# Optimization experiments

Hardware: AMD Instinct MI355X
Metric: run time of the kernel (lower is better)

Reference implementation:

```python
import jax, jax.numpy as jnp
import numpy as np

B, T, E, A, S, H = 1024, 64, 1024, 10, 30, 200  # batch, time, embed, actdim, stoch, deter==hidden
MIN_STD = 0.1


def _xavier(key, fan_in, fan_out):
    lim = float(np.sqrt(6.0 / (fan_in + fan_out)))
    return jax.random.uniform(key, (fan_in, fan_out), jnp.float32, -lim, lim)


def setup_inputs() -> dict:
    key = jax.random.key(0)
    ks = jax.random.split(key, 20)
    gl = 1.0 / float(np.sqrt(H))  # torch GRUCell default init bound
    inp = {
        'embed': jax.random.normal(ks[0], (B, T, E), jnp.float32),
        'action': jax.random.normal(ks[1], (B, T, A), jnp.float32),
        'eps_post': jax.random.normal(ks[2], (T, B, S), jnp.float32),
        'eps_prior': jax.random.normal(ks[3], (T, B, S), jnp.float32),
        # Linear weights stored [in, out] (transposed vs torch) so x @ W works.
        'img1_w': _xavier(ks[4], A + S, H), 'img1_b': jnp.zeros((H,), jnp.float32),
        'gru_wi': jax.random.uniform(ks[5], (H, 3 * H), jnp.float32, -gl, gl),
        'gru_wh': jax.random.uniform(ks[6], (H, 3 * H), jnp.float32, -gl, gl),
        'gru_bi': jax.random.uniform(ks[7], (3 * H,), jnp.float32, -gl, gl),
        'gru_bh': jax.random.uniform(ks[8], (3 * H,), jnp.float32, -gl, gl),
        'img2_w': _xavier(ks[9], H, H), 'img2_b': jnp.zeros((H,), jnp.float32),
        'img3_w': _xavier(ks[10], H, 2 * S), 'img3_b': jnp.zeros((2 * S,), jnp.float32),
        'obs1_w': _xavier(ks[11], H + E, H), 'obs1_b': jnp.zeros((H,), jnp.float32),
        'obs2_w': _xavier(ks[12], H, 2 * S), 'obs2_b': jnp.zeros((2 * S,), jnp.float32),
    }
    return inp


def _observe(embed, action, eps_post, eps_prior,
             img1_w, img1_b, gru_wi, gru_wh, gru_bi, gru_bh,
             img2_w, img2_b, img3_w, img3_b, obs1_w, obs1_b, obs2_w, obs2_b):
    elu = jax.nn.elu
    embed_t = jnp.transpose(embed, (1, 0, 2))   # [T,B,E]
    action_t = jnp.transpose(action, (1, 0, 2))  # [T,B,A]

    def step(carry, xs):
        stoch, deter = carry
        a, emb, ep_q, ep_p = xs
        # img_step (prior)
        x = elu(jnp.concatenate([stoch, a], -1) @ img1_w + img1_b)
        gi = x @ gru_wi + gru_bi
        gh = deter @ gru_wh + gru_bh
        ir, iz, i_n = jnp.split(gi, 3, axis=-1)
        hr, hz, h_n = jnp.split(gh, 3, axis=-1)
        r = jax.nn.sigmoid(ir + hr)
        z = jax.nn.sigmoid(iz + hz)
        n = jnp.tanh(i_n + r * h_n)
        deter = (1.0 - z) * n + z * deter
        y = elu(deter @ img2_w + img2_b) @ img3_w + img3_b
        p_mean, p_std = jnp.split(y, 2, axis=-1)
        p_std = jax.nn.softplus(p_std) + MIN_STD
        p_stoch = p_mean + p_std * ep_p  # rsample
        # obs_step (posterior)
        o = elu(jnp.concatenate([deter, emb], -1) @ obs1_w + obs1_b) @ obs2_w + obs2_b
        q_mean, q_std = jnp.split(o, 2, axis=-1)
        q_std = jax.nn.softplus(q_std) + MIN_STD
        q_stoch = q_mean + q_std * ep_q  # rsample
        out = jnp.concatenate([q_mean, q_std, q_stoch, deter,
                               p_mean, p_std, p_stoch, deter], axis=-1)
        return (q_stoch, deter), out

    init = (jnp.zeros((B, S), embed.dtype), jnp.zeros((B, H), embed.dtype))
    _, outs = jax.lax.scan(step, init, (action_t, embed_t, eps_post, eps_prior))
    # outs: [T, B, 2*(3S+H)] -> [B, T, 580]; layout: post(mean,std,stoch,deter)|prior(mean,std,stoch,deter)
    return jnp.transpose(outs, (1, 0, 2))


def reference(embed, action, eps_post, eps_prior,
              img1_w, img1_b, gru_wi, gru_wh, gru_bi, gru_bh,
              img2_w, img2_b, img3_w, img3_b, obs1_w, obs1_b, obs2_w, obs2_b):
    return _observe(embed, action, eps_post, eps_prior,
                    img1_w, img1_b, gru_wi, gru_wh, gru_bi, gru_bh,
                    img2_w, img2_b, img3_w, img3_b, obs1_w, obs1_b, obs2_w, obs2_b)
```

## Files before the change

### kernel.cpp

```cpp
#include <hip/hip_runtime.h>

#define T_ 64

typedef __attribute__((ext_vector_type(4))) float f32x4;
typedef __attribute__((ext_vector_type(8))) short s16x8;

__device__ __forceinline__ unsigned short f2bf(float f) {
  unsigned u = __float_as_uint(f);
  u = (u + 0x7FFFu + ((u >> 16) & 1u)) >> 16;
  return (unsigned short)u;
}
__device__ __forceinline__ float bf2f(unsigned short h) {
  return __uint_as_float(((unsigned)h) << 16);
}
__device__ __forceinline__ float eluf(float x) { return x > 0.f ? x : __expf(x) - 1.f; }
__device__ __forceinline__ float sigmf(float x) { return 1.f / (1.f + __expf(-x)); }
__device__ __forceinline__ float tanh_(float x) {
  float xx = fminf(fmaxf(x, -30.f), 30.f);
  float e = __expf(-2.f * xx);
  return (1.f - e) / (1.f + e);
}
__device__ __forceinline__ float softpf(float x) {
  return x > 20.f ? x : __logf(1.f + __expf(x));
}

#define OPW1   0
#define OPWI   6656
#define OPWH   126464
#define OPO1D  246272
#define OPO2   286208
#define OPI2   298496
#define OPI3   345088
#define OWIWT  359424
#define OWHWT  364416
#define OO1DWT 369408
#define OI1WT  371072
#define OO2WT  372736
#define PK_U16 373248

#define OFF_PK  26214400
#define OFF_SWZ 26960896

__device__ void pack_mat(int idx, int stride, const float* __restrict__ W,
                         int K, int N, int KT, int NT, unsigned short* __restrict__ dst) {
  int total = KT * NT * 512;
  for (int i = idx; i < total; i += stride) {
    int j = i & 7, l = (i >> 3) & 63, rem = i >> 9;
    int kt = rem % KT, nt = rem / KT;
    int n = nt * 16 + (l & 15), k = kt * 32 + (l >> 4) * 8 + j;
    float v = (k < K && n < N) ? W[(size_t)k * N + n] : 0.f;
    dst[i] = f2bf(v);
  }
}

__device__ void pack_gate(int idx, int stride, const float* __restrict__ W,
                          unsigned short* __restrict__ dst) {
  int total = 3 * 13 * 6 * 512;
  for (int i = idx; i < total; i += stride) {
    int j = i & 7, l = (i >> 3) & 63, rem = i >> 9;
    int kt = rem % 6, rem2 = rem / 6, nt = rem2 % 13, g = rem2 / 13;
    int u = nt * 16 + (l & 15);
    int k = kt * 32 + (l >> 4) * 8 + j;
    float v = (u < 200) ? W[(size_t)k * 600 + g * 200 + u] : 0.f;
    dst[i] = f2bf(v);
  }
}

__global__ void prep_weights(const float* __restrict__ w1, const float* __restrict__ wi,
                             const float* __restrict__ wh, const float* __restrict__ i2,
                             const float* __restrict__ i3, const float* __restrict__ obs1w,
                             const float* __restrict__ o2,
                             unsigned short* __restrict__ pk,
                             unsigned short* __restrict__ swz) {
  int idx = blockIdx.x * blockDim.x + threadIdx.x;
  int stride = gridDim.x * blockDim.x;
  pack_mat(idx, stride, w1, 40, 200, 1, 13, pk + OPW1);
  pack_gate(idx, stride, wi, pk + OPWI);
  pack_gate(idx, stride, wh, pk + OPWH);
  pack_mat(idx, stride, obs1w, 200, 200, 6, 13, pk + OPO1D);
  pack_mat(idx, stride, o2, 200, 60, 6, 4, pk + OPO2);
  pack_mat(idx, stride, i2, 200, 200, 7, 13, pk + OPI2);
  pack_mat(idx, stride, i3, 200, 60, 7, 4, pk + OPI3);
  for (int i = idx; i < 4992; i += stride) {
    int j = i & 7, c = (i >> 3) % 208, g = i / 1664;
    pk[OWIWT + i] = f2bf((c < 200) ? wi[(size_t)(192 + j) * 600 + g * 200 + c] : 0.f);
    pk[OWHWT + i] = f2bf((c < 200) ? wh[(size_t)(192 + j) * 600 + g * 200 + c] : 0.f);
  }
  for (int i = idx; i < 1664; i += stride) {
    int c = i >> 3, j = i & 7;
    pk[OO1DWT + i] = f2bf((c < 200) ? obs1w[(size_t)(192 + j) * 200 + c] : 0.f);
    pk[OI1WT + i]  = f2bf((c < 200) ? w1[(size_t)(32 + j) * 200 + c] : 0.f);
  }
  for (int i = idx; i < 512; i += stride) {
    int c = i >> 3, j = i & 7;
    pk[OO2WT + i] = f2bf((c < 60) ? o2[(size_t)(192 + j) * 60 + c] : 0.f);
  }
  for (int i = idx; i < 212992; i += stride) {
    int j = i & 7, l = (i >> 3) & 63, rem = i >> 9;
    int nt = rem % 13, kc = rem / 13;
    int k = kc * 32 + ((l >> 4) * 8) + j;
    int n = nt * 16 + (l & 15);
    float v = (n < 200) ? obs1w[(size_t)(200 + k) * 200 + n] : 0.0f;
    swz[i] = f2bf(v);
  }
}

__global__ __launch_bounds__(256) void emb_gemm(const float* __restrict__ embed,
                                                const float* __restrict__ obs1b,
                                                const unsigned short* __restrict__ swz,
                                                unsigned short* __restrict__ emb_pre) {
  __shared__ __align__(16) unsigned short lds_A[64][40];
  int tid = threadIdx.x;
  int lane = tid & 63, w = tid >> 6;
  int R0 = blockIdx.x * 64;
  int tt = R0 >> 10;
  int bb = R0 & 1023;

  f32x4 acc[13];
#pragma unroll
  for (int nt = 0; nt < 13; ++nt) acc[nt] = (f32x4){0.f, 0.f, 0.f, 0.f};

  int i_row = tid >> 2, cg = tid & 3;
  const float* arow = embed + ((size_t)(bb + i_row) * 64 + tt) * 1024 + cg * 8;

  for (int kc = 0; kc < 32; ++kc) {
    __syncthreads();
    {
      const float* p = arow + kc * 32;
      f32x4 a0 = *(const f32x4*)p;
      f32x4 a1 = *(const f32x4*)(p + 4);
      unsigned short* dst = &lds_A[i_row][cg * 8];
      dst[0] = f2bf(a0[0]); dst[1] = f2bf(a0[1]); dst[2] = f2bf(a0[2]); dst[3] = f2bf(a0[3]);
      dst[4] = f2bf(a1[0]); dst[5] = f2bf(a1[1]); dst[6] = f2bf(a1[2]); dst[7] = f2bf(a1[3]);
    }
    __syncthreads();
    s16x8 af = *(const s16x8*)&lds_A[w * 16 + (lane & 15)][(lane >> 4) * 8];
    const unsigned short* bp = swz + (size_t)kc * 6656 + (size_t)lane * 8;
#pragma unroll
    for (int nt = 0; nt < 13; ++nt) {
      s16x8 bfv = *(const s16x8*)(bp + nt * 512);
      acc[nt] = __builtin_amdgcn_mfma_f32_16x16x32_bf16(af, bfv, acc[nt], 0, 0, 0);
    }
  }
  int r0 = R0 + w * 16 + ((lane >> 4) << 2);
  int c0 = lane & 15;
#pragma unroll
  for (int nt = 0; nt < 13; ++nt) {
    int n = nt * 16 + c0;
    if (n < 200) {
      float bv = obs1b[n];
#pragma unroll
      for (int rr = 0; rr < 4; ++rr)
        emb_pre[(size_t)(r0 + rr) * 200 + n] = f2bf(acc[nt][rr] + bv);
    }
  }
}

#define LGKM0  asm volatile("s_waitcnt lgkmcnt(0)" ::: "memory")
#define MEMCLB asm volatile("" ::: "memory")
#define BAR()  __builtin_amdgcn_s_barrier()
#define MFMA16(A, B, C) __builtin_amdgcn_mfma_f32_16x16x32_bf16((A), (B), (C), 0, 0, 0)
#define WV9  asm volatile("s_waitcnt vmcnt(9)" ::: "memory")
#define WV29 asm volatile("s_waitcnt vmcnt(29)" ::: "memory")
#define WV4  asm volatile("s_waitcnt vmcnt(4)" ::: "memory")
#define WV0  asm volatile("s_waitcnt vmcnt(0)" ::: "memory")

typedef __attribute__((address_space(3))) unsigned int u32_lds;
typedef const __attribute__((address_space(1))) unsigned int u32_glb;

__device__ __forceinline__ void gll16(const unsigned short* g, unsigned short* l, int lane) {
  __builtin_amdgcn_global_load_lds((u32_glb*)(g + lane * 8), (u32_lds*)l, 16, 0, 0);
}

template <int TB, bool BIGB>
__device__ __forceinline__ f32x4 cons6(const s16x8* A, f32x4 acc,
                                       unsigned short* ringw, const unsigned* toffw,
                                       const unsigned short* pk, int lane) {
#pragma unroll
  for (int kt = 0; kt < 6; ++kt) {
    const int tau = TB + kt;
    if ((tau & 3) == 0) {
      if (tau < 8) { if (BIGB) { WV29; } else { WV9; } }
      else { WV4; }
    }
    s16x8 Bv = *(const s16x8*)(ringw + (tau & 7) * 512 + lane * 8);
    acc = MFMA16(A[kt], Bv, acc);
    if ((tau & 3) == 3) {
      LGKM0; MEMCLB;
#pragma unroll
      for (int k2 = 1; k2 <= 4; ++k2) {
        const int tile = (tau + 4 + k2) % 48;
        gll16(pk + toffw[tile], ringw + (tile & 7) * 512, lane);
      }
      MEMCLB;
    }
  }
  return acc;
}

__device__ __forceinline__ f32x4 res6(const s16x8* A, const s16x8* Wt, f32x4 acc) {
#pragma unroll
  for (int kt = 0; kt < 6; ++kt) acc = MFMA16(A[kt], Wt[kt], acc);
  return acc;
}
__device__ __forceinline__ f32x4 rem1(const s16x8& A6, const unsigned short* wt,
                                      const unsigned short* zb, bool kg0, f32x4 acc) {
  const unsigned short* p = kg0 ? wt : zb;
  return MFMA16(A6, *(const s16x8*)p, acc);
}
__device__ __forceinline__ void grustep(const f32x4& rv, const f32x4& zv,
                                        const f32x4& inv, const f32x4& hnv, f32x4& dv) {
#pragma unroll
  for (int rr = 0; rr < 4; ++rr) {
    float r = sigmf(rv[rr]);
    float z = sigmf(zv[rr]);
    float n = tanh_(inv[rr] + r * hnv[rr]);
    dv[rr] = (1.f - z) * n + z * dv[rr];
  }
}

__global__ __launch_bounds__(512, 1) void scan_v7(
    const float* __restrict__ action, const float* __restrict__ eps_post,
    const float* __restrict__ img1_b, const float* __restrict__ gru_bi,
    const float* __restrict__ gru_bh, const float* __restrict__ obs2_b,
    const unsigned short* __restrict__ pk, const unsigned short* __restrict__ emb_pre,
    float* __restrict__ out) {

  __shared__ __align__(16) unsigned short ring[8][8][512];
  __shared__ __align__(16) unsigned short l_w1[13 * 512];
  __shared__ __align__(16) unsigned short l_wiWT[3][208][8];
  __shared__ __align__(16) unsigned short l_whWT[3][208][8];
  __shared__ __align__(16) unsigned short l_o1dWT[208][8];
  __shared__ __align__(16) unsigned short l_i1WT[208][8];
  __shared__ __align__(16) unsigned short l_o2WT[64][8];
  __shared__ __align__(16) unsigned short zblk[8];
  __shared__ __align__(16) unsigned short xoA[28][16][8];
  __shared__ __align__(16) unsigned short dA[28][16][8];
  __shared__ __align__(16) unsigned short sA[8][16][8];
  __shared__ __align__(16) float s_o[60][20];
  __shared__ __align__(16) float outbuf[16][292];
  __shared__ unsigned l_toff[8][48];

  const int tid = threadIdx.x, lane = tid & 63, w = tid >> 6;
  const int arow = lane & 15, kg = lane >> 4;
  const bool kg0 = (kg == 0);
  const int b0 = blockIdx.x * 16;
  unsigned short* ringw = &ring[w][0][0];
  const unsigned* toffw = &l_toff[w][0];

  for (int i = tid; i < 28 * 16 * 8; i += 512) { (&xoA[0][0][0])[i] = 0; (&dA[0][0][0])[i] = 0; }
  for (int i = tid; i < 8 * 16 * 8; i += 512) (&sA[0][0][0])[i] = 0;
  for (int i = tid; i < 13 * 512; i += 512) l_w1[i] = pk[OPW1 + i];
  for (int i = tid; i < 4992; i += 512) {
    (&l_wiWT[0][0][0])[i] = pk[OWIWT + i];
    (&l_whWT[0][0][0])[i] = pk[OWHWT + i];
  }
  for (int i = tid; i < 1664; i += 512) {
    (&l_o1dWT[0][0])[i] = pk[OO1DWT + i];
    (&l_i1WT[0][0])[i] = pk[OI1WT + i];
  }
  for (int i = tid; i < 512; i += 512) (&l_o2WT[0][0])[i] = pk[OO2WT + i];
  if (tid < 8) zblk[tid] = 0;
  for (int i = tid; i < 8 * 48; i += 512) {
    int ww = i / 48, tau = i % 48;
    unsigned off;
    if (ww < 5) {
      if (tau < 18) { int g = tau / 6, kt = tau % 6; off = OPWI + ((g * 13 + ww) * 6 + kt) * 512; }
      else {
        int t2 = tau - 18, ug = ww + 8;
        if (t2 < 6)       off = OPWI + ((0 * 13 + ug) * 6 + t2) * 512;
        else if (t2 < 12) off = OPWI + ((1 * 13 + ug) * 6 + (t2 - 6)) * 512;
        else if (t2 < 18) off = OPWH + ((1 * 13 + ug) * 6 + (t2 - 12)) * 512;
        else if (t2 < 24) off = OPWI + ((2 * 13 + ug) * 6 + (t2 - 18)) * 512;
        else              off = OPWH + ((2 * 13 + ug) * 6 + (t2 - 24)) * 512;
      }
    } else {
      if (tau < 18) { int g = tau / 6, kt = tau % 6; off = OPWI + ((g * 13 + ww) * 6 + kt) * 512; }
      else if (tau < 42) {
        int i4 = (tau - 18) / 6, kt = (tau - 18) % 6;
        int nt = (ww - 5) * 4 + i4;
        off = OPO1D + (nt * 6 + kt) * 512;
      } else {
        int kt = tau - 42;
        int nt5 = (ww == 5) ? 0 : (ww == 6) ? 1 : 3;
        off = OPO2 + (nt5 * 6 + kt) * 512;
      }
    }
    l_toff[ww][tau] = off;
  }

  s16x8 wB[4][6];
  {
    const unsigned short* base[4];
    if (w < 5) {
      base[0] = pk + OPWH + (size_t)((0 * 13 + w) * 6) * 512;
      base[1] = pk + OPWH + (size_t)((1 * 13 + w) * 6) * 512;
      base[2] = pk + OPWH + (size_t)((2 * 13 + w) * 6) * 512;
      base[3] = pk + OPWH + (size_t)((0 * 13 + w + 8) * 6) * 512;
    } else {
      base[0] = pk + OPWH + (size_t)((0 * 13 + w) * 6) * 512;
      base[1] = pk + OPWH + (size_t)((1 * 13 + w) * 6) * 512;
      base[2] = pk + OPWH + (size_t)((2 * 13 + w) * 6) * 512;
      if (w == 5)      base[3] = pk + OPO1D + (size_t)(12 * 6) * 512;
      else if (w == 7) base[3] = pk + OPO2 + (size_t)(2 * 6) * 512;
      else             base[3] = pk + OPO1D;
    }
#pragma unroll
    for (int s = 0; s < 4; ++s)
#pragma unroll
      for (int kt = 0; kt < 6; ++kt)
        wB[s][kt] = *(const s16x8*)(base[s] + (size_t)kt * 512 + lane * 8);
  }

  const int uA = w * 16 + arow;
  const int uB = (w + 8) * 16 + arow;
  const bool mB = (w < 5) && (uB < 200);
  const int uBc = (uB < 200) ? uB : 199;
  float bsA0 = gru_bi[uA] + gru_bh[uA];
  float bsA1 = gru_bi[200 + uA] + gru_bh[200 + uA];
  float bi2a = gru_bi[400 + uA], bh2a = gru_bh[400 + uA];
  float bsB0 = mB ? (gru_bi[uBc] + gru_bh[uBc]) : 0.f;
  float bsB1 = mB ? (gru_bi[200 + uBc] + gru_bh[200 + uBc]) : 0.f;
  float bi2b = mB ? gru_bi[400 + uBc] : 0.f;
  float bh2b = mB ? gru_bh[400 + uBc] : 0.f;
  float b1A = img1_b[uA];
  float b1B = mB ? img1_b[uBc] : 0.f;
  float b5a = 0.f, b5b = 0.f;
  if (w == 5) b5a = obs2_b[arow];
  else if (w == 6) b5a = obs2_b[16 + arow];
  else if (w == 7) { b5a = (48 + arow < 60) ? obs2_b[48 + arow] : 0.f; b5b = obs2_b[32 + arow]; }

  unsigned short e16[20];
#pragma unroll
  for (int i = 0; i < 20; ++i) e16[i] = 0;
  if (w >= 5) {
#pragma unroll
    for (int i = 0; i < 5; ++i) {
      int nt = (w == 5) ? ((i < 4) ? i : 12) : ((w == 6) ? (4 + ((i < 4) ? i : 3)) : (8 + ((i < 4) ? i : 3)));
      int c = nt * 16 + arow; int cc = (c < 200) ? c : 199;
#pragma unroll
      for (int rr = 0; rr < 4; ++rr)
        e16[i * 4 + rr] = emb_pre[((size_t)(b0 + kg * 4 + rr)) * 200 + cc];
    }
  }
  float epsv;
  { int it = (tid < 480) ? tid : 479;
    epsv = eps_post[((size_t)(b0 + it / 30)) * 30 + it % 30]; }
  float act0, actn;
  { int sl = (lane < 20) ? (w * 20 + lane) : (w * 20);
    act0 = action[((size_t)(b0 + sl / 10) * T_ + 0) * 10 + sl % 10];
    actn = action[((size_t)(b0 + sl / 10) * T_ + 1) * 10 + sl % 10]; }
  f32x4 dv0 = {0.f, 0.f, 0.f, 0.f}, dv1 = {0.f, 0.f, 0.f, 0.f};

  __syncthreads();
  if (lane < 20) {
    int sl = w * 20 + lane; int kk = sl % 10, r = sl / 10;
    sA[(30 + kk) >> 3][r][(30 + kk) & 7] = f2bf(act0);
  }
#pragma unroll
  for (int tt = 0; tt < 8; ++tt) gll16(pk + toffw[tt], ringw + tt * 512, lane);
  WV0;
  __syncthreads();

  for (int t = 0; t < T_; ++t) {
    {
      s16x8 a0 = *(const s16x8*)&sA[kg][arow][0];
      s16x8 a1 = *(const s16x8*)&sA[4 + kg][arow][0];
      {
        s16x8 B0 = *(const s16x8*)&l_w1[w * 512 + lane * 8];
        f32x4 acc = {b1A, b1A, b1A, b1A};
        acc = MFMA16(a0, B0, acc);
        acc = rem1(a1, &l_i1WT[uA][0], zblk, kg0, acc);
#pragma unroll
        for (int rr = 0; rr < 4; ++rr)
          xoA[uA >> 3][kg * 4 + rr][uA & 7] = f2bf(eluf(acc[rr]));
      }
      if (w < 5) {
        s16x8 B0 = *(const s16x8*)&l_w1[(w + 8) * 512 + lane * 8];
        f32x4 acc = {b1B, b1B, b1B, b1B};
        acc = MFMA16(a0, B0, acc);
        acc = rem1(a1, &l_i1WT[uB][0], zblk, kg0, acc);
        if (uB < 200) {
#pragma unroll
          for (int rr = 0; rr < 4; ++rr)
            xoA[uB >> 3][kg * 4 + rr][uB & 7] = f2bf(eluf(acc[rr]));
        }
      }
    }
    LGKM0; BAR();

    {
      s16x8 ax[6], ad[6];
#pragma unroll
      for (int kt = 0; kt < 6; ++kt) {
        ax[kt] = *(const s16x8*)&xoA[kt * 4 + kg][arow][0];
        ad[kt] = *(const s16x8*)&dA[kt * 4 + kg][arow][0];
      }
      s16x8 ax6 = *(const s16x8*)&xoA[24 + kg][arow][0];
      s16x8 ad6 = *(const s16x8*)&dA[24 + kg][arow][0];
      if (w < 5) {
        f32x4 rv = cons6<0, false>(ax, (f32x4){bsA0, bsA0, bsA0, bsA0}, ringw, toffw, pk, lane);
        rv = rem1(ax6, &l_wiWT[0][uA][0], zblk, kg0, rv);
        rv = res6(ad, wB[0], rv);
        rv = rem1(ad6, &l_whWT[0][uA][0], zblk, kg0, rv);
        f32x4 zv = cons6<6, false>(ax, (f32x4){bsA1, bsA1, bsA1, bsA1}, ringw, toffw, pk, lane);
        zv = rem1(ax6, &l_wiWT[1][uA][0], zblk, kg0, zv);
        zv = res6(ad, wB[1], zv);
        zv = rem1(ad6, &l_whWT[1][uA][0], zblk, kg0, zv);
        f32x4 inv = cons6<12, false>(ax, (f32x4){bi2a, bi2a, bi2a, bi2a}, ringw, toffw, pk, lane);
        inv = rem1(ax6, &l_wiWT[2][uA][0], zblk, kg0, inv);
        f32x4 hnv = res6(ad, wB[2], (f32x4){bh2a, bh2a, bh2a, bh2a});
        hnv = rem1(ad6, &l_whWT[2][uA][0], zblk, kg0, hnv);
        grustep(rv, zv, inv, hnv, dv0);
#pragma unroll
        for (int rr = 0; rr < 4; ++rr) outbuf[kg * 4 + rr][90 + uA] = dv0[rr];
        f32x4 rv2 = cons6<18, false>(ax, (f32x4){bsB0, bsB0, bsB0, bsB0}, ringw, toffw, pk, lane);
        rv2 = rem1(ax6, &l_wiWT[0][uB][0], zblk, kg0, rv2);
        rv2 = res6(ad, wB[3], rv2);
        rv2 = rem1(ad6, &l_whWT[0][uB][0], zblk, kg0, rv2);
        f32x4 zv2 = cons6<24, false>(ax, (f32x4){bsB1, bsB1, bsB1, bsB1}, ringw, toffw, pk, lane);
        zv2 = cons6<30, false>(ad, zv2, ringw, toffw, pk, lane);
        zv2 = rem1(ax6, &l_wiWT[1][uB][0], zblk, kg0, zv2);
        zv2 = rem1(ad6, &l_whWT[1][uB][0], zblk, kg0, zv2);
        f32x4 inv2 = cons6<36, false>(ax, (f32x4){bi2b, bi2b, bi2b, bi2b}, ringw, toffw, pk, lane);
        inv2 = rem1(ax6, &l_wiWT[2][uB][0], zblk, kg0, inv2);
        f32x4 hnv2 = cons6<42, false>(ad, (f32x4){bh2b, bh2b, bh2b, bh2b}, ringw, toffw, pk, lane);
        hnv2 = rem1(ad6, &l_whWT[2][uB][0], zblk, kg0, hnv2);
        grustep(rv2, zv2, inv2, hnv2, dv1);
        if (uB < 200) {
#pragma unroll
          for (int rr = 0; rr < 4; ++rr) outbuf[kg * 4 + rr][90 + uB] = dv1[rr];
        }
      } else {
        f32x4 rv = cons6<0, true>(ax, (f32x4){bsA0, bsA0, bsA0, bsA0}, ringw, toffw, pk, lane);
        rv = rem1(ax6, &l_wiWT[0][uA][0], zblk, kg0, rv);
        rv = res6(ad, wB[0], rv);
        rv = rem1(ad6, &l_whWT[0][uA][0], zblk, kg0, rv);
        f32x4 zv = cons6<6, true>(ax, (f32x4){bsA1, bsA1, bsA1, bsA1}, ringw, toffw, pk, lane);
        zv = rem1(ax6, &l_wiWT[1][uA][0], zblk, kg0, zv);
        zv = res6(ad, wB[1], zv);
        zv = rem1(ad6, &l_whWT[1][uA][0], zblk, kg0, zv);
        f32x4 inv = cons6<12, true>(ax, (f32x4){bi2a, bi2a, bi2a, bi2a}, ringw, toffw, pk, lane);
        inv = rem1(ax6, &l_wiWT[2][uA][0], zblk, kg0, inv);
        f32x4 hnv = res6(ad, wB[2], (f32x4){bh2a, bh2a, bh2a, bh2a});
        hnv = rem1(ad6, &l_whWT[2][uA][0], zblk, kg0, hnv);
        grustep(rv, zv, inv, hnv, dv0);
#pragma unroll
        for (int rr = 0; rr < 4; ++rr) outbuf[kg * 4 + rr][90 + uA] = dv0[rr];
      }
    }
    LGKM0; BAR();

    {
#pragma unroll
      for (int rr = 0; rr < 4; ++rr)
        dA[uA >> 3][kg * 4 + rr][uA & 7] = f2bf(dv0[rr]);
      if (mB) {
#pragma unroll
        for (int rr = 0; rr < 4; ++rr)
          dA[uB >> 3][kg * 4 + rr][uB & 7] = f2bf(dv1[rr]);
      }
    }
    LGKM0; BAR();

    if (w >= 5) {
      s16x8 ad4[6];
#pragma unroll
      for (int kt = 0; kt < 6; ++kt) ad4[kt] = *(const s16x8*)&dA[kt * 4 + kg][arow][0];
      s16x8 ad46 = *(const s16x8*)&dA[24 + kg][arow][0];
      const int ntb = (w - 5) * 4;
      {
        int c = (ntb + 0) * 16 + arow;
        f32x4 acc = cons6<18, true>(ad4, (f32x4){0.f, 0.f, 0.f, 0.f}, ringw, toffw, pk, lane);
        acc = rem1(ad46, &l_o1dWT[c][0], zblk, kg0, acc);
#pragma unroll
        for (int rr = 0; rr < 4; ++rr)
          xoA[c >> 3][kg * 4 + rr][c & 7] = f2bf(eluf(acc[rr] + bf2f(e16[0 * 4 + rr])));
      }
      {
        int c = (ntb + 1) * 16 + arow;
        f32x4 acc = cons6<24, true>(ad4, (f32x4){0.f, 0.f, 0.f, 0.f}, ringw, toffw, pk, lane);
        acc = rem1(ad46, &l_o1dWT[c][0], zblk, kg0, acc);
#pragma unroll
        for (int rr = 0; rr < 4; ++rr)
          xoA[c >> 3][kg * 4 + rr][c & 7] = f2bf(eluf(acc[rr] + bf2f(e16[1 * 4 + rr])));
      }
      {
        int c = (ntb + 2) * 16 + arow;
        f32x4 acc = cons6<30, true>(ad4, (f32x4){0.f, 0.f, 0.f, 0.f}, ringw, toffw, pk, lane);
        acc = rem1(ad46, &l_o1dWT[c][0], zblk, kg0, acc);
#pragma unroll
        for (int rr = 0; rr < 4; ++rr)
          xoA[c >> 3][kg * 4 + rr][c & 7] = f2bf(eluf(acc[rr] + bf2f(e16[2 * 4 + rr])));
      }
      {
        int c = (ntb + 3) * 16 + arow;
        f32x4 acc = cons6<36, true>(ad4, (f32x4){0.f, 0.f, 0.f, 0.f}, ringw, toffw, pk, lane);
        acc = rem1(ad46, &l_o1dWT[c][0], zblk, kg0, acc);
#pragma unroll
        for (int rr = 0; rr < 4; ++rr)
          xoA[c >> 3][kg * 4 + rr][c & 7] = f2bf(eluf(acc[rr] + bf2f(e16[3 * 4 + rr])));
      }
      if (w == 5) {
        int c = 192 + arow;
        f32x4 acc = res6(ad4, wB[3], (f32x4){0.f, 0.f, 0.f, 0.f});
        acc = rem1(ad46, &l_o1dWT[c][0], zblk, kg0, acc);
        if (c < 200) {
#pragma unroll
          for (int rr = 0; rr < 4; ++rr)
            xoA[c >> 3][kg * 4 + rr][c & 7] = f2bf(eluf(acc[rr] + bf2f(e16[16 + rr])));
        }
      }
    }
    LGKM0; BAR();

    if (w >= 5) {
      s16x8 a5[6];
#pragma unroll
      for (int kt = 0; kt < 6; ++kt) a5[kt] = *(const s16x8*)&xoA[kt * 4 + kg][arow][0];
      s16x8 a56 = *(const s16x8*)&xoA[24 + kg][arow][0];
      int c5 = (w == 5) ? arow : (w == 6) ? (16 + arow) : (48 + arow);
      f32x4 acc = cons6<42, true>(a5, (f32x4){b5a, b5a, b5a, b5a}, ringw, toffw, pk, lane);
      {
        int c5c = (c5 < 64) ? c5 : 63;
        acc = rem1(a56, &l_o2WT[c5c][0], zblk, kg0, acc);
      }
      if (c5 < 60) *(f32x4*)&s_o[c5][kg * 4] = acc;
      if (w == 7) {
        int c5r = 32 + arow;
        f32x4 acc2 = res6(a5, wB[3], (f32x4){b5b, b5b, b5b, b5b});
        acc2 = rem1(a56, &l_o2WT[c5r][0], zblk, kg0, acc2);
        *(f32x4*)&s_o[c5r][kg * 4] = acc2;
      }
    }
    LGKM0; BAR();

    MEMCLB;
    {
      if (tid < 480) {
        int r = tid / 30, j = tid % 30;
        float qm = s_o[j][r];
        float qs = softpf(s_o[j + 30][r]) + 0.1f;
        float qst = qm + qs * epsv;
        outbuf[r][j] = qm; outbuf[r][30 + j] = qs; outbuf[r][60 + j] = qst;
        sA[j >> 3][r][j & 7] = f2bf(qst);
      }
      if (lane < 20) {
        int sl = w * 20 + lane; int kk = sl % 10, r = sl / 10;
        sA[(30 + kk) >> 3][r][(30 + kk) & 7] = f2bf(actn);
      }
      int tc = (t + 1 < T_) ? t + 1 : T_ - 1;
      int ta = (t + 2 < T_) ? t + 2 : T_ - 1;
      MEMCLB;
      if (w >= 5) {
#pragma unroll
        for (int i = 0; i < 5; ++i) {
          int nt = (w == 5) ? ((i < 4) ? i : 12) : ((w == 6) ? (4 + ((i < 4) ? i : 3)) : (8 + ((i < 4) ? i : 3)));
          int c = nt * 16 + arow; int cc = (c < 200) ? c : 199;
#pragma unroll
          for (int rr = 0; rr < 4; ++rr)
            e16[i * 4 + rr] = emb_pre[((size_t)tc * 1024 + b0 + kg * 4 + rr) * 200 + cc];
        }
      }
      { int it = (tid < 480) ? tid : 479;
        epsv = eps_post[((size_t)tc * 1024 + b0 + it / 30) * 30 + it % 30]; }
      { int sl = (lane < 20) ? (w * 20 + lane) : (w * 20);
        actn = action[((size_t)(b0 + sl / 10) * T_ + ta) * 10 + sl % 10]; }
      MEMCLB;
    }
    LGKM0; BAR();

#pragma unroll
    for (int k2 = 0; k2 < 3; ++k2) {
      int idx = tid + k2 * 512; idx = (idx < 1168) ? idx : 1167;
      int row = idx / 73, ci = idx - row * 73;
      f32x4 v = *(const f32x4*)&outbuf[row][ci * 4];
      *(f32x4*)(out + ((size_t)(b0 + row) * T_ + t) * 580 + ci * 4) = v;
    }
    MEMCLB;
  }
}

__global__ __launch_bounds__(256) void post_head(const float* __restrict__ eps_prior,
                                                 const float* __restrict__ img2_b,
                                                 const float* __restrict__ img3_b,
                                                 const unsigned short* __restrict__ pk,
                                                 float* __restrict__ out) {
  __shared__ __align__(16) unsigned short dAp[4][28][16][8];
  __shared__ __align__(16) unsigned short y1p[4][28][16][8];
  __shared__ __align__(16) float s_p[60][68];
  int b = blockIdx.x;
  int tid = threadIdx.x;
  int lane = tid & 63, w = tid >> 6, arow = lane & 15, kg = lane >> 4;

  for (int i = tid; i < 1536; i += 256) {
    int mt = i / 384, rem = i % 384;
    int gidx = 25 + rem / 128, r2 = (rem % 128) / 8, j = rem & 7;
    dAp[mt][gidx][r2][j] = 0;
    y1p[mt][gidx][r2][j] = 0;
  }
  for (int i = tid; i < 12800; i += 256) {
    int row = i / 200, c = i % 200;
    float v = out[((size_t)(b * 64 + row)) * 580 + 90 + c];
    dAp[row >> 4][c >> 3][row & 15][c & 7] = f2bf(v);
  }
  __syncthreads();

  s16x8 ad[7];
#pragma unroll
  for (int kt = 0; kt < 7; ++kt) ad[kt] = *(const s16x8*)&dAp[w][kt * 4 + kg][arow][0];
#pragma unroll
  for (int nt = 0; nt < 13; ++nt) {
    int col = nt * 16 + arow;
    float bv = (col < 200) ? img2_b[col] : 0.f;
    f32x4 acc = {bv, bv, bv, bv};
#pragma unroll
    for (int kt = 0; kt < 7; ++kt) {
      s16x8 Bv = *(const s16x8*)(pk + OPI2 + (size_t)((nt * 7 + kt) * 512) + lane * 8);
      acc = __builtin_amdgcn_mfma_f32_16x16x32_bf16(ad[kt], Bv, acc, 0, 0, 0);
    }
    if (col < 200) {
#pragma unroll
      for (int rr = 0; rr < 4; ++rr)
        y1p[w][col >> 3][kg * 4 + rr][col & 7] = f2bf(eluf(acc[rr]));
    }
  }
  __syncthreads();

  s16x8 ay[7];
#pragma unroll
  for (int kt = 0; kt < 7; ++kt) ay[kt] = *(const s16x8*)&y1p[w][kt * 4 + kg][arow][0];
#pragma unroll
  for (int nt = 0; nt < 4; ++nt) {
    int col = nt * 16 + arow;
    float bv = (col < 60) ? img3_b[col] : 0.f;
    f32x4 acc = {bv, bv, bv, bv};
#pragma unroll
    for (int kt = 0; kt < 7; ++kt) {
      s16x8 Bv = *(const s16x8*)(pk + OPI3 + (size_t)((nt * 7 + kt) * 512) + lane * 8);
      acc = __builtin_amdgcn_mfma_f32_16x16x32_bf16(ay[kt], Bv, acc, 0, 0, 0);
    }
    if (col < 60) {
#pragma unroll
      for (int rr = 0; rr < 4; ++rr) s_p[col][w * 16 + kg * 4 + rr] = acc[rr];
    }
  }
  __syncthreads();

  for (int i = tid; i < 1920; i += 256) {
    int row = i / 30, j = i % 30;
    float pm = s_p[j][row];
    float ps = softpf(s_p[j + 30][row]) + 0.1f;
    float pst = pm + ps * eps_prior[((size_t)row * 1024 + b) * 30 + j];
    size_t ob = ((size_t)b * 64 + row) * 580;
    out[ob + 290 + j] = pm;
    out[ob + 320 + j] = ps;
    out[ob + 350 + j] = pst;
  }
  for (int i = tid; i < 6400; i += 256) {
    int row = i / 100, c2 = i % 100;
    size_t ob = ((size_t)b * 64 + row) * 580;
    *(float2*)&out[ob + 380 + c2 * 2] = *(const float2*)&out[ob + 90 + c2 * 2];
  }
}

extern "C" void kernel_launch(void* const* d_in, const int* in_sizes, int n_in,
                              void* d_out, int out_size, void* d_ws, size_t ws_size,
                              hipStream_t stream) {
  const float* embed    = (const float*)d_in[0];
  const float* action   = (const float*)d_in[1];
  const float* eps_post = (const float*)d_in[2];
  const float* eps_prior= (const float*)d_in[3];
  const float* img1_w   = (const float*)d_in[4];
  const float* img1_b   = (const float*)d_in[5];
  const float* gru_wi   = (const float*)d_in[6];
  const float* gru_wh   = (const float*)d_in[7];
  const float* gru_bi   = (const float*)d_in[8];
  const float* gru_bh   = (const float*)d_in[9];
  const float* img2_w   = (const float*)d_in[10];
  const float* img2_b   = (const float*)d_in[11];
  const float* img3_w   = (const float*)d_in[12];
  const float* img3_b   = (const float*)d_in[13];
  const float* obs1_w   = (const float*)d_in[14];
  const float* obs1_b   = (const float*)d_in[15];
  const float* obs2_w   = (const float*)d_in[16];
  const float* obs2_b   = (const float*)d_in[17];

  char* ws = (char*)d_ws;
  unsigned short* emb_pre = (unsigned short*)ws;
  unsigned short* pkw     = (unsigned short*)(ws + OFF_PK);
  unsigned short* swz     = (unsigned short*)(ws + OFF_SWZ);
  float* outp = (float*)d_out;

  prep_weights<<<256, 256, 0, stream>>>(img1_w, gru_wi, gru_wh, img2_w, img3_w,
                                        obs1_w, obs2_w, pkw, swz);
  emb_gemm<<<1024, 256, 0, stream>>>(embed, obs1_b, swz, emb_pre);
  scan_v7<<<64, 512, 0, stream>>>(action, eps_post, img1_b, gru_bi, gru_bh,
                                  obs2_b, pkw, emb_pre, outp);
  post_head<<<1024, 256, 0, stream>>>(eps_prior, img2_b, img3_b, pkw, outp);
}
```

Before: 1.067 ms.

## Restart weight ring prefetch each step and use nontemporal loads/stores

Changes the streamed-weight ring pipeline. The ring no longer wraps tiles across timesteps modulo 48. It stops issuing prefetches past tile 47, drains fully at tile 44, and issues the first 8 tiles again at the end of each timestep, overlapping them with the output store. Per-step inputs and output stores now use nontemporal builtins to reduce cache pollution, and out-of-range uB indices are clamped for the LDS weight reads. The simpler vmcnt accounting may expose weight-load latency at the start of each step.

```diff
diff --git a/kernel.cpp b/kernel.cpp
--- a/kernel.cpp
+++ b/kernel.cpp
@@ -160,8 +160,7 @@
 #define MEMCLB asm volatile("" ::: "memory")
 #define BAR()  __builtin_amdgcn_s_barrier()
 #define MFMA16(A, B, C) __builtin_amdgcn_mfma_f32_16x16x32_bf16((A), (B), (C), 0, 0, 0)
-#define WV9  asm volatile("s_waitcnt vmcnt(9)" ::: "memory")
-#define WV29 asm volatile("s_waitcnt vmcnt(29)" ::: "memory")
+#define WV8  asm volatile("s_waitcnt vmcnt(8)" ::: "memory")
 #define WV4  asm volatile("s_waitcnt vmcnt(4)" ::: "memory")
 #define WV0  asm volatile("s_waitcnt vmcnt(0)" ::: "memory")
 
@@ -172,7 +171,7 @@
   __builtin_amdgcn_global_load_lds((u32_glb*)(g + lane * 8), (u32_lds*)l, 16, 0, 0);
 }
 
-template <int TB, bool BIGB>
+template <int TB>
 __device__ __forceinline__ f32x4 cons6(const s16x8* A, f32x4 acc,
                                        unsigned short* ringw, const unsigned* toffw,
                                        const unsigned short* pk, int lane) {
@@ -180,8 +179,7 @@
   for (int kt = 0; kt < 6; ++kt) {
     const int tau = TB + kt;
     if ((tau & 3) == 0) {
-      if (tau < 8) { if (BIGB) { WV29; } else { WV9; } }
-      else { WV4; }
+      if (tau == 44) { WV0; } else { WV4; }
     }
     s16x8 Bv = *(const s16x8*)(ringw + (tau & 7) * 512 + lane * 8);
     acc = MFMA16(A[kt], Bv, acc);
@@ -189,8 +187,8 @@
       LGKM0; MEMCLB;
 #pragma unroll
       for (int k2 = 1; k2 <= 4; ++k2) {
-        const int tile = (tau + 4 + k2) % 48;
-        gll16(pk + toffw[tile], ringw + (tile & 7) * 512, lane);
+        const int raw = tau + 4 + k2;
+        if (raw < 48) gll16(pk + toffw[raw], ringw + (raw & 7) * 512, lane);
       }
       MEMCLB;
     }
@@ -219,7 +217,7 @@
   }
 }
 
-__global__ __launch_bounds__(512, 1) void scan_v7(
+__global__ __launch_bounds__(512, 1) void scan_v9(
     const float* __restrict__ action, const float* __restrict__ eps_post,
     const float* __restrict__ img1_b, const float* __restrict__ gru_bi,
     const float* __restrict__ gru_bh, const float* __restrict__ obs2_b,
@@ -340,16 +338,16 @@
       int c = nt * 16 + arow; int cc = (c < 200) ? c : 199;
 #pragma unroll
       for (int rr = 0; rr < 4; ++rr)
-        e16[i * 4 + rr] = emb_pre[((size_t)(b0 + kg * 4 + rr)) * 200 + cc];
+        e16[i * 4 + rr] = __builtin_nontemporal_load(&emb_pre[((size_t)(b0 + kg * 4 + rr)) * 200 + cc]);
     }
   }
   float epsv;
   { int it = (tid < 480) ? tid : 479;
-    epsv = eps_post[((size_t)(b0 + it / 30)) * 30 + it % 30]; }
+    epsv = __builtin_nontemporal_load(&eps_post[((size_t)(b0 + it / 30)) * 30 + it % 30]); }
   float act0, actn;
   { int sl = (lane < 20) ? (w * 20 + lane) : (w * 20);
-    act0 = action[((size_t)(b0 + sl / 10) * T_ + 0) * 10 + sl % 10];
-    actn = action[((size_t)(b0 + sl / 10) * T_ + 1) * 10 + sl % 10]; }
+    act0 = __builtin_nontemporal_load(&action[((size_t)(b0 + sl / 10) * T_ + 0) * 10 + sl % 10]);
+    actn = __builtin_nontemporal_load(&action[((size_t)(b0 + sl / 10) * T_ + 1) * 10 + sl % 10]); }
   f32x4 dv0 = {0.f, 0.f, 0.f, 0.f}, dv1 = {0.f, 0.f, 0.f, 0.f};
 
   __syncthreads();
@@ -379,7 +377,7 @@
         s16x8 B0 = *(const s16x8*)&l_w1[(w + 8) * 512 + lane * 8];
         f32x4 acc = {b1B, b1B, b1B, b1B};
         acc = MFMA16(a0, B0, acc);
-        acc = rem1(a1, &l_i1WT[uB][0], zblk, kg0, acc);
+        acc = rem1(a1, &l_i1WT[uBc][0], zblk, kg0, acc);
         if (uB < 200) {
 #pragma unroll
           for (int rr = 0; rr < 4; ++rr)
@@ -399,48 +397,48 @@
       s16x8 ax6 = *(const s16x8*)&xoA[24 + kg][arow][0];
       s16x8 ad6 = *(const s16x8*)&dA[24 + kg][arow][0];
       if (w < 5) {
-        f32x4 rv = cons6<0, false>(ax, (f32x4){bsA0, bsA0, bsA0, bsA0}, ringw, toffw, pk, lane);
+        f32x4 rv = cons6<0>(ax, (f32x4){bsA0, bsA0, bsA0, bsA0}, ringw, toffw, pk, lane);
         rv = rem1(ax6, &l_wiWT[0][uA][0], zblk, kg0, rv);
         rv = res6(ad, wB[0], rv);
         rv = rem1(ad6, &l_whWT[0][uA][0], zblk, kg0, rv);
-        f32x4 zv = cons6<6, false>(ax, (f32x4){bsA1, bsA1, bsA1, bsA1}, ringw, toffw, pk, lane);
+        f32x4 zv = cons6<6>(ax, (f32x4){bsA1, bsA1, bsA1, bsA1}, ringw, toffw, pk, lane);
         zv = rem1(ax6, &l_wiWT[1][uA][0], zblk, kg0, zv);
         zv = res6(ad, wB[1], zv);
         zv = rem1(ad6, &l_whWT[1][uA][0], zblk, kg0, zv);
-        f32x4 inv = cons6<12, false>(ax, (f32x4){bi2a, bi2a, bi2a, bi2a}, ringw, toffw, pk, lane);
+        f32x4 inv = cons6<12>(ax, (f32x4){bi2a, bi2a, bi2a, bi2a}, ringw, toffw, pk, lane);
         inv = rem1(ax6, &l_wiWT[2][uA][0], zblk, kg0, inv);
         f32x4 hnv = res6(ad, wB[2], (f32x4){bh2a, bh2a, bh2a, bh2a});
         hnv = rem1(ad6, &l_whWT[2][uA][0], zblk, kg0, hnv);
         grustep(rv, zv, inv, hnv, dv0);
 #pragma unroll
         for (int rr = 0; rr < 4; ++rr) outbuf[kg * 4 + rr][90 + uA] = dv0[rr];
-        f32x4 rv2 = cons6<18, false>(ax, (f32x4){bsB0, bsB0, bsB0, bsB0}, ringw, toffw, pk, lane);
-        rv2 = rem1(ax6, &l_wiWT[0][uB][0], zblk, kg0, rv2);
+        f32x4 rv2 = cons6<18>(ax, (f32x4){bsB0, bsB0, bsB0, bsB0}, ringw, toffw, pk, lane);
+        rv2 = rem1(ax6, &l_wiWT[0][uBc][0], zblk, kg0, rv2);
         rv2 = res6(ad, wB[3], rv2);
-        rv2 = rem1(ad6, &l_whWT[0][uB][0], zblk, kg0, rv2);
-        f32x4 zv2 = cons6<24, false>(ax, (f32x4){bsB1, bsB1, bsB1, bsB1}, ringw, toffw, pk, lane);
-        zv2 = cons6<30, false>(ad, zv2, ringw, toffw, pk, lane);
-        zv2 = rem1(ax6, &l_wiWT[1][uB][0], zblk, kg0, zv2);
-        zv2 = rem1(ad6, &l_whWT[1][uB][0], zblk, kg0, zv2);
-        f32x4 inv2 = cons6<36, false>(ax, (f32x4){bi2b, bi2b, bi2b, bi2b}, ringw, toffw, pk, lane);
-        inv2 = rem1(ax6, &l_wiWT[2][uB][0], zblk, kg0, inv2);
-        f32x4 hnv2 = cons6<42, false>(ad, (f32x4){bh2b, bh2b, bh2b, bh2b}, ringw, toffw, pk, lane);
-        hnv2 = rem1(ad6, &l_whWT[2][uB][0], zblk, kg0, hnv2);
+        rv2 = rem1(ad6, &l_whWT[0][uBc][0], zblk, kg0, rv2);
+        f32x4 zv2 = cons6<24>(ax, (f32x4){bsB1, bsB1, bsB1, bsB1}, ringw, toffw, pk, lane);
+        zv2 = cons6<30>(ad, zv2, ringw, toffw, pk, lane);
+        zv2 = rem1(ax6, &l_wiWT[1][uBc][0], zblk, kg0, zv2);
+        zv2 = rem1(ad6, &l_whWT[1][uBc][0], zblk, kg0, zv2);
+        f32x4 inv2 = cons6<36>(ax, (f32x4){bi2b, bi2b, bi2b, bi2b}, ringw, toffw, pk, lane);
+        inv2 = rem1(ax6, &l_wiWT[2][uBc][0], zblk, kg0, inv2);
+        f32x4 hnv2 = cons6<42>(ad, (f32x4){bh2b, bh2b, bh2b, bh2b}, ringw, toffw, pk, lane);
+        hnv2 = rem1(ad6, &l_whWT[2][uBc][0], zblk, kg0, hnv2);
         grustep(rv2, zv2, inv2, hnv2, dv1);
         if (uB < 200) {
 #pragma unroll
           for (int rr = 0; rr < 4; ++rr) outbuf[kg * 4 + rr][90 + uB] = dv1[rr];
         }
       } else {
-        f32x4 rv = cons6<0, true>(ax, (f32x4){bsA0, bsA0, bsA0, bsA0}, ringw, toffw, pk, lane);
+        f32x4 rv = cons6<0>(ax, (f32x4){bsA0, bsA0, bsA0, bsA0}, ringw, toffw, pk, lane);
         rv = rem1(ax6, &l_wiWT[0][uA][0], zblk, kg0, rv);
         rv = res6(ad, wB[0], rv);
         rv = rem1(ad6, &l_whWT[0][uA][0], zblk, kg0, rv);
-        f32x4 zv = cons6<6, true>(ax, (f32x4){bsA1, bsA1, bsA1, bsA1}, ringw, toffw, pk, lane);
+        f32x4 zv = cons6<6>(ax, (f32x4){bsA1, bsA1, bsA1, bsA1}, ringw, toffw, pk, lane);
         zv = rem1(ax6, &l_wiWT[1][uA][0], zblk, kg0, zv);
         zv = res6(ad, wB[1], zv);
         zv = rem1(ad6, &l_whWT[1][uA][0], zblk, kg0, zv);
-        f32x4 inv = cons6<12, true>(ax, (f32x4){bi2a, bi2a, bi2a, bi2a}, ringw, toffw, pk, lane);
+        f32x4 inv = cons6<12>(ax, (f32x4){bi2a, bi2a, bi2a, bi2a}, ringw, toffw, pk, lane);
         inv = rem1(ax6, &l_wiWT[2][uA][0], zblk, kg0, inv);
         f32x4 hnv = res6(ad, wB[2], (f32x4){bh2a, bh2a, bh2a, bh2a});
         hnv = rem1(ad6, &l_whWT[2][uA][0], zblk, kg0, hnv);
@@ -471,35 +469,35 @@
       const int ntb = (w - 5) * 4;
       {
         int c = (ntb + 0) * 16 + arow;
-        f32x4 acc = cons6<18, true>(ad4, (f32x4){0.f, 0.f, 0.f, 0.f}, ringw, toffw, pk, lane);
+        f32x4 acc = cons6<18>(ad4, (f32x4){0.f, 0.f, 0.f, 0.f}, ringw, toffw, pk, lane);
         acc = rem1(ad46, &l_o1dWT[c][0], zblk, kg0, acc);
 #pragma unroll
         for (int rr = 0; rr < 4; ++rr)
-          xoA[c >> 3][kg * 4 + rr][c & 7] = f2bf(eluf(acc[rr] + bf2f(e16[0 * 4 + rr])));
+          xoA[c >> 3][kg * 4 + rr][c & 7] = f2bf(eluf(acc[rr] + bf2f(e16[0 + rr])));
       }
       {
         int c = (ntb + 1) * 16 + arow;
-        f32x4 acc = cons6<24, true>(ad4, (f32x4){0.f, 0.f, 0.f, 0.f}, ringw, toffw, pk, lane);
+        f32x4 acc = cons6<24>(ad4, (f32x4){0.f, 0.f, 0.f, 0.f}, ringw, toffw, pk, lane);
         acc = rem1(ad46, &l_o1dWT[c][0], zblk, kg0, acc);
 #pragma unroll
         for (int rr = 0; rr < 4; ++rr)
-          xoA[c >> 3][kg * 4 + rr][c & 7] = f2bf(eluf(acc[rr] + bf2f(e16[1 * 4 + rr])));
+          xoA[c >> 3][kg * 4 + rr][c & 7] = f2bf(eluf(acc[rr] + bf2f(e16[4 + rr])));
       }
       {
         int c = (ntb + 2) * 16 + arow;
-        f32x4 acc = cons6<30, true>(ad4, (f32x4){0.f, 0.f, 0.f, 0.f}, ringw, toffw, pk, lane);
+        f32x4 acc = cons6<30>(ad4, (f32x4){0.f, 0.f, 0.f, 0.f}, ringw, toffw, pk, lane);
         acc = rem1(ad46, &l_o1dWT[c][0], zblk, kg0, acc);
 #pragma unroll
         for (int rr = 0; rr < 4; ++rr)
-          xoA[c >> 3][kg * 4 + rr][c & 7] = f2bf(eluf(acc[rr] + bf2f(e16[2 * 4 + rr])));
+          xoA[c >> 3][kg * 4 + rr][c & 7] = f2bf(eluf(acc[rr] + bf2f(e16[8 + rr])));
       }
       {
         int c = (ntb + 3) * 16 + arow;
-        f32x4 acc = cons6<36, true>(ad4, (f32x4){0.f, 0.f, 0.f, 0.f}, ringw, toffw, pk, lane);
+        f32x4 acc = cons6<36>(ad4, (f32x4){0.f, 0.f, 0.f, 0.f}, ringw, toffw, pk, lane);
         acc = rem1(ad46, &l_o1dWT[c][0], zblk, kg0, acc);
 #pragma unroll
         for (int rr = 0; rr < 4; ++rr)
-          xoA[c >> 3][kg * 4 + rr][c & 7] = f2bf(eluf(acc[rr] + bf2f(e16[3 * 4 + rr])));
+          xoA[c >> 3][kg * 4 + rr][c & 7] = f2bf(eluf(acc[rr] + bf2f(e16[12 + rr])));
       }
       if (w == 5) {
         int c = 192 + arow;
@@ -520,7 +518,7 @@
       for (int kt = 0; kt < 6; ++kt) a5[kt] = *(const s16x8*)&xoA[kt * 4 + kg][arow][0];
       s16x8 a56 = *(const s16x8*)&xoA[24 + kg][arow][0];
       int c5 = (w == 5) ? arow : (w == 6) ? (16 + arow) : (48 + arow);
-      f32x4 acc = cons6<42, true>(a5, (f32x4){b5a, b5a, b5a, b5a}, ringw, toffw, pk, lane);
+      f32x4 acc = cons6<42>(a5, (f32x4){b5a, b5a, b5a, b5a}, ringw, toffw, pk, lane);
       {
         int c5c = (c5 < 64) ? c5 : 63;
         acc = rem1(a56, &l_o2WT[c5c][0], zblk, kg0, acc);
@@ -559,13 +557,16 @@
           int c = nt * 16 + arow; int cc = (c < 200) ? c : 199;
 #pragma unroll
           for (int rr = 0; rr < 4; ++rr)
-            e16[i * 4 + rr] = emb_pre[((size_t)tc * 1024 + b0 + kg * 4 + rr) * 200 + cc];
+            e16[i * 4 + rr] = __builtin_nontemporal_load(
+                &emb_pre[((size_t)tc * 1024 + b0 + kg * 4 + rr) * 200 + cc]);
         }
       }
       { int it = (tid < 480) ? tid : 479;
-        epsv = eps_post[((size_t)tc * 1024 + b0 + it / 30) * 30 + it % 30]; }
+        epsv = __builtin_nontemporal_load(
+            &eps_post[((size_t)tc * 1024 + b0 + it / 30) * 30 + it % 30]); }
       { int sl = (lane < 20) ? (w * 20 + lane) : (w * 20);
-        actn = action[((size_t)(b0 + sl / 10) * T_ + ta) * 10 + sl % 10]; }
+        actn = __builtin_nontemporal_load(
+            &action[((size_t)(b0 + sl / 10) * T_ + ta) * 10 + sl % 10]); }
       MEMCLB;
     }
     LGKM0; BAR();
@@ -575,8 +576,12 @@
       int idx = tid + k2 * 512; idx = (idx < 1168) ? idx : 1167;
       int row = idx / 73, ci = idx - row * 73;
       f32x4 v = *(const f32x4*)&outbuf[row][ci * 4];
-      *(f32x4*)(out + ((size_t)(b0 + row) * T_ + t) * 580 + ci * 4) = v;
-    }
+      __builtin_nontemporal_store(v, (f32x4*)(out + ((size_t)(b0 + row) * T_ + t) * 580 + ci * 4));
+    }
+    MEMCLB;
+#pragma unroll
+    for (int tt = 0; tt < 8; ++tt) gll16(pk + toffw[tt], ringw + tt * 512, lane);
+    WV8;
     MEMCLB;
   }
 }
@@ -695,7 +700,7 @@
   prep_weights<<<256, 256, 0, stream>>>(img1_w, gru_wi, gru_wh, img2_w, img3_w,
                                         obs1_w, obs2_w, pkw, swz);
   emb_gemm<<<1024, 256, 0, stream>>>(embed, obs1_b, swz, emb_pre);
-  scan_v7<<<64, 512, 0, stream>>>(action, eps_post, img1_b, gru_bi, gru_bh,
+  scan_v9<<<64, 512, 0, stream>>>(action, eps_post, img1_b, gru_bi, gru_bh,
                                   obs2_b, pkw, emb_pre, outp);
   post_head<<<1024, 256, 0, stream>>>(eps_prior, img2_b, img3_b, pkw, outp);
 }
```

New measurement: 1.094 ms. 1.03x slower.
